# Optimization experiments

Measured on AMD Instinct MI355X. Metric: run time of the kernel, lower is better.

Reference implementation:

```python
import jax, jax.numpy as jnp
import numpy as np


def setup_inputs() -> dict:
    key = jax.random.key(0)
    k1, k2 = jax.random.split(key)
    B, HW, C, M, P = 8, 4096, 1024, 32, 512
    feature_map = jax.random.normal(k1, (B, HW, C), dtype=jnp.float32)
    # normalized (y, x) coords in [0,1], as produced by mask.nonzero()/[H,W]
    point_coords = jax.random.uniform(k2, (B, M, P, 2), dtype=jnp.float32)
    return {"feature_map": feature_map, "point_coords": point_coords}


def reference(feature_map, point_coords):
    # feature_map: [B, H*W, C]; point_coords: [B, M, P, 2] as (y_norm, x_norm).
    B, HW, C = feature_map.shape
    h = w = int(np.sqrt(HW))
    # torch flips coords to (x, y); grid_sample(align_corners=True) maps
    # grid g = 2*coord-1 to pixel coord*(size-1).
    y = point_coords[..., 0] * (h - 1)  # [B, M, P]
    x = point_coords[..., 1] * (w - 1)
    x0f = jnp.floor(x)
    y0f = jnp.floor(y)
    wx = (x - x0f)[..., None]  # [B, M, P, 1]
    wy = (y - y0f)[..., None]
    ix0 = jnp.clip(x0f.astype(jnp.int32), 0, w - 1)
    ix1 = jnp.clip(ix0 + 1, 0, w - 1)
    iy0 = jnp.clip(y0f.astype(jnp.int32), 0, h - 1)
    iy1 = jnp.clip(iy0 + 1, 0, h - 1)

    def gather(iy, ix):
        idx = (iy * w + ix).reshape(B, -1)  # [B, M*P]
        g = jnp.take_along_axis(feature_map, idx[:, :, None], axis=1)  # [B, M*P, C]
        return g.reshape(B, iy.shape[1], iy.shape[2], C)

    f00 = gather(iy0, ix0)
    f01 = gather(iy0, ix1)
    f10 = gather(iy1, ix0)
    f11 = gather(iy1, ix1)
    # bilinear interpolation -> [B, M, P, C]
    sampled = (f00 * (1 - wx) * (1 - wy) + f01 * wx * (1 - wy)
               + f10 * (1 - wx) * wy + f11 * wx * wy)
    # AdaptiveAvgPool1d(1) over points, then transpose -> [B, M, 1, C]
    region_feat = jnp.mean(sampled, axis=2, keepdims=True)
    return region_feat
```

## Files before the change

### kernel.cpp

```cpp
#include <hip/hip_runtime.h>


#define NB 8
#define NM 32
#define NP 512
#define NC 1024
#define NH 64
#define NHW 4096

#define KC   256
#define NKC  (NHW / KC)
#define CT   256
#define NCT  (NC / CT)
#define PF   8

__global__ __launch_bounds__(256) void scatter_w(
    const float* __restrict__ pc, float* __restrict__ W)
{
    int idx = blockIdx.x * 256 + threadIdx.x;
    int bm  = idx >> 9;
    int m   = bm & (NM - 1);
    int b   = bm >> 5;

    float2 c = ((const float2*)pc)[idx];
    float y = c.x * 63.0f;
    float x = c.y * 63.0f;
    float x0f = floorf(x), y0f = floorf(y);
    float wx = x - x0f, wy = y - y0f;
    int ix0 = min(max((int)x0f, 0), 63);
    int ix1 = min(ix0 + 1, 63);
    int iy0 = min(max((int)y0f, 0), 63);
    int iy1 = min(iy0 + 1, 63);
    float wx1 = 1.0f - wx, wy1 = 1.0f - wy;
    const float s = 1.0f / (float)NP;

    float* Wb = W + (size_t)b * (NHW * NM) + m;
    atomicAdd(Wb + ((iy0 * NH + ix0) * NM), wx1 * wy1 * s);
    atomicAdd(Wb + ((iy0 * NH + ix1) * NM), wx  * wy1 * s);
    atomicAdd(Wb + ((iy1 * NH + ix0) * NM), wx1 * wy  * s);
    atomicAdd(Wb + ((iy1 * NH + ix1) * NM), wx  * wy  * s);
}

__global__ __launch_bounds__(256, 2) void wgemm(
    const float* __restrict__ W, const float* __restrict__ F,
    float* __restrict__ P)
{
    __shared__ float4 sW[KC * NM / 4];

    const int kc  = blockIdx.x;
    const int ct  = blockIdx.y;
    const int b   = blockIdx.z;
    const int tid = threadIdx.x;
    const int c   = ct * CT + tid;
    const int hw0 = kc * KC;

    const float4* Wg = (const float4*)(W + ((size_t)b * NHW + hw0) * NM);
#pragma unroll
    for (int j = 0; j < 8; ++j)
        sW[tid + 256 * j] = Wg[tid + 256 * j];
    __syncthreads();

    const float* Fb = F + ((size_t)b * NHW + hw0) * NC + c;

    float acc[NM];
#pragma unroll
    for (int m = 0; m < NM; ++m) acc[m] = 0.0f;

    float fbuf[PF];
#pragma unroll
    for (int j = 0; j < PF; ++j) fbuf[j] = Fb[(size_t)j * NC];

    for (int i = 0; i < KC; i += PF) {
        float fcur[PF];
#pragma unroll
        for (int j = 0; j < PF; ++j) fcur[j] = fbuf[j];
        if (i + PF < KC) {
#pragma unroll
            for (int j = 0; j < PF; ++j)
                fbuf[j] = Fb[(size_t)(i + PF + j) * NC];
        }
#pragma unroll
        for (int j = 0; j < PF; ++j) {
            const float4* w4 = sW + (i + j) * (NM / 4);
            float f = fcur[j];
#pragma unroll
            for (int mq = 0; mq < NM / 4; ++mq) {
                float4 w = w4[mq];
                acc[mq * 4 + 0] = fmaf(w.x, f, acc[mq * 4 + 0]);
                acc[mq * 4 + 1] = fmaf(w.y, f, acc[mq * 4 + 1]);
                acc[mq * 4 + 2] = fmaf(w.z, f, acc[mq * 4 + 2]);
                acc[mq * 4 + 3] = fmaf(w.w, f, acc[mq * 4 + 3]);
            }
        }
    }

    float* pb = P + (((size_t)kc * NB + b) * NM) * NC + c;
#pragma unroll
    for (int m = 0; m < NM; ++m)
        pb[(size_t)m * NC] = acc[m];
}

__global__ __launch_bounds__(256) void reduce_p(
    const float* __restrict__ P, float* __restrict__ out)
{
    const int idx = blockIdx.x * 256 + threadIdx.x;
    const float4* p4 = (const float4*)P;
    const int stride = NB * NM * NC / 4;
    float4 s = make_float4(0.f, 0.f, 0.f, 0.f);
#pragma unroll
    for (int kc = 0; kc < NKC; ++kc) {
        float4 v = p4[(size_t)kc * stride + idx];
        s.x += v.x; s.y += v.y; s.z += v.z; s.w += v.w;
    }
    ((float4*)out)[idx] = s;
}

__global__ __launch_bounds__(256) void region_pool_direct(
    const float* __restrict__ fm, const float* __restrict__ pc,
    float* __restrict__ out)
{
    __shared__ int4   sIdx[NP];
    __shared__ float4 sWt[NP];
    const int bid = blockIdx.x;
    const int b   = bid >> 5;
    const int tid = threadIdx.x;
    const float2* pc2 = (const float2*)(pc + (size_t)bid * NP * 2);
    for (int p = tid; p < NP; p += 256) {
        float2 c = pc2[p];
        float y = c.x * 63.0f, x = c.y * 63.0f;
        float x0f = floorf(x), y0f = floorf(y);
        float wx = x - x0f, wy = y - y0f;
        int ix0 = min(max((int)x0f, 0), 63);
        int ix1 = min(ix0 + 1, 63);
        int iy0 = min(max((int)y0f, 0), 63);
        int iy1 = min(iy0 + 1, 63);
        sIdx[p] = make_int4((iy0 * NH + ix0) << 10, (iy0 * NH + ix1) << 10,
                            (iy1 * NH + ix0) << 10, (iy1 * NH + ix1) << 10);
        float wx1 = 1.0f - wx, wy1 = 1.0f - wy;
        sWt[p] = make_float4(wx1 * wy1, wx * wy1, wx1 * wy, wx * wy);
    }
    __syncthreads();
    const float* Fb = fm + (size_t)b * (NHW * NC) + tid * 4;
    float4 acc = make_float4(0.f, 0.f, 0.f, 0.f);
#pragma unroll 4
    for (int p = 0; p < NP; ++p) {
        int4 off = sIdx[p]; float4 w = sWt[p];
        float4 f00 = *(const float4*)(Fb + off.x);
        float4 f01 = *(const float4*)(Fb + off.y);
        float4 f10 = *(const float4*)(Fb + off.z);
        float4 f11 = *(const float4*)(Fb + off.w);
        acc.x = fmaf(w.x, f00.x, fmaf(w.y, f01.x, fmaf(w.z, f10.x, fmaf(w.w, f11.x, acc.x))));
        acc.y = fmaf(w.x, f00.y, fmaf(w.y, f01.y, fmaf(w.z, f10.y, fmaf(w.w, f11.y, acc.y))));
        acc.z = fmaf(w.x, f00.z, fmaf(w.y, f01.z, fmaf(w.z, f10.z, fmaf(w.w, f11.z, acc.z))));
        acc.w = fmaf(w.x, f00.w, fmaf(w.y, f01.w, fmaf(w.z, f10.w, fmaf(w.w, f11.w, acc.w))));
    }
    const float inv = 1.0f / (float)NP;
    ((float4*)(out + (size_t)bid * NC))[tid] =
        make_float4(acc.x * inv, acc.y * inv, acc.z * inv, acc.w * inv);
}

extern "C" void kernel_launch(void* const* d_in, const int* in_sizes, int n_in,
                              void* d_out, int out_size, void* d_ws, size_t ws_size,
                              hipStream_t stream) {
    const float* fm = (const float*)d_in[0];
    const float* pc = (const float*)d_in[1];
    float* out = (float*)d_out;

    const size_t wbytes = (size_t)NB * NHW * NM * sizeof(float);
    const size_t pbytes = (size_t)NKC * NB * NM * NC * sizeof(float);
    if (ws_size >= wbytes + pbytes) {
        float* W = (float*)d_ws;
        float* P = (float*)((char*)d_ws + wbytes);
        hipMemsetAsync(W, 0, wbytes, stream);
        scatter_w<<<(NB * NM * NP) / 256, 256, 0, stream>>>(pc, W);
        dim3 grid(NKC, NCT, NB);
        wgemm<<<grid, CT, 0, stream>>>(W, fm, P);
        reduce_p<<<(NB * NM * NC / 4) / 256, 256, 0, stream>>>(P, out);
    } else {
        region_pool_direct<<<NB * NM, 256, 0, stream>>>(fm, pc, out);
    }
}
```

Before: 233.1 us.

## Retile wgemm into per-wave 8x8 register tiles with float4 feature loads

Restructures the weighted-GEMM kernel so each wave owns 8 regions and each thread accumulates 8 channels via two float4 loads. Feature reads move from scalar to vectorized loads, and the weight reads per FMA from LDS fall. The HW chunk shrinks to 128 with a deeper occupancy hint, which doubles the partial sums that reduce_p must combine. Each block's four waves now re-read the same feature rows, relying on cache.

```diff
diff --git a/kernel.cpp b/kernel.cpp
--- a/kernel.cpp
+++ b/kernel.cpp
@@ -8,11 +8,10 @@
 #define NH 64
 #define NHW 4096
 
-#define KC   256
+#define KC   128
 #define NKC  (NHW / KC)
-#define CT   256
-#define NCT  (NC / CT)
-#define PF   8
+#define NCT  2
+#define PF   2
 
 __global__ __launch_bounds__(256) void scatter_w(
     const float* __restrict__ pc, float* __restrict__ W)
@@ -41,63 +40,136 @@
     atomicAdd(Wb + ((iy1 * NH + ix1) * NM), wx  * wy  * s);
 }
 
-__global__ __launch_bounds__(256, 2) void wgemm(
+__global__ __launch_bounds__(256, 4) void wgemm(
     const float* __restrict__ W, const float* __restrict__ F,
     float* __restrict__ P)
 {
     __shared__ float4 sW[KC * NM / 4];
 
-    const int kc  = blockIdx.x;
-    const int ct  = blockIdx.y;
-    const int b   = blockIdx.z;
-    const int tid = threadIdx.x;
-    const int c   = ct * CT + tid;
-    const int hw0 = kc * KC;
+    const int kc   = blockIdx.x;
+    const int ct   = blockIdx.y;
+    const int b    = blockIdx.z;
+    const int tid  = threadIdx.x;
+    const int wav  = tid >> 6;
+    const int lane = tid & 63;
+    const int c0   = ct * 512 + lane * 4;
+    const int hw0  = kc * KC;
+    const int wq   = wav * 2;
 
     const float4* Wg = (const float4*)(W + ((size_t)b * NHW + hw0) * NM);
 #pragma unroll
-    for (int j = 0; j < 8; ++j)
+    for (int j = 0; j < 4; ++j)
         sW[tid + 256 * j] = Wg[tid + 256 * j];
     __syncthreads();
 
-    const float* Fb = F + ((size_t)b * NHW + hw0) * NC + c;
-
-    float acc[NM];
-#pragma unroll
-    for (int m = 0; m < NM; ++m) acc[m] = 0.0f;
-
-    float fbuf[PF];
-#pragma unroll
-    for (int j = 0; j < PF; ++j) fbuf[j] = Fb[(size_t)j * NC];
+    const float* Fb = F + ((size_t)b * NHW + hw0) * NC + c0;
+
+    float4 acc[8][2];
+#pragma unroll
+    for (int m = 0; m < 8; ++m) {
+        acc[m][0] = make_float4(0.f, 0.f, 0.f, 0.f);
+        acc[m][1] = make_float4(0.f, 0.f, 0.f, 0.f);
+    }
+
+    float4 fb0[PF], fb1[PF];
+#pragma unroll
+    for (int j = 0; j < PF; ++j) {
+        fb0[j] = *(const float4*)(Fb + (size_t)j * NC);
+        fb1[j] = *(const float4*)(Fb + (size_t)j * NC + 256);
+    }
 
     for (int i = 0; i < KC; i += PF) {
-        float fcur[PF];
-#pragma unroll
-        for (int j = 0; j < PF; ++j) fcur[j] = fbuf[j];
-        if (i + PF < KC) {
-#pragma unroll
-            for (int j = 0; j < PF; ++j)
-                fbuf[j] = Fb[(size_t)(i + PF + j) * NC];
+#pragma unroll
+        for (int j = 0; j < PF; ++j) {
+            float4 f0 = fb0[j], f1 = fb1[j];
+            int inx = i + PF + j;
+            if (inx < KC) {
+                fb0[j] = *(const float4*)(Fb + (size_t)inx * NC);
+                fb1[j] = *(const float4*)(Fb + (size_t)inx * NC + 256);
+            }
+            float4 wa = sW[(i + j) * 8 + wq];
+            float4 wb = sW[(i + j) * 8 + wq + 1];
+
+            acc[0][0].x = fmaf(wa.x, f0.x, acc[0][0].x);
+            acc[0][0].y = fmaf(wa.x, f0.y, acc[0][0].y);
+            acc[0][0].z = fmaf(wa.x, f0.z, acc[0][0].z);
+            acc[0][0].w = fmaf(wa.x, f0.w, acc[0][0].w);
+            acc[0][1].x = fmaf(wa.x, f1.x, acc[0][1].x);
+            acc[0][1].y = fmaf(wa.x, f1.y, acc[0][1].y);
+            acc[0][1].z = fmaf(wa.x, f1.z, acc[0][1].z);
+            acc[0][1].w = fmaf(wa.x, f1.w, acc[0][1].w);
+
+            acc[1][0].x = fmaf(wa.y, f0.x, acc[1][0].x);
+            acc[1][0].y = fmaf(wa.y, f0.y, acc[1][0].y);
+            acc[1][0].z = fmaf(wa.y, f0.z, acc[1][0].z);
+            acc[1][0].w = fmaf(wa.y, f0.w, acc[1][0].w);
+            acc[1][1].x = fmaf(wa.y, f1.x, acc[1][1].x);
+            acc[1][1].y = fmaf(wa.y, f1.y, acc[1][1].y);
+            acc[1][1].z = fmaf(wa.y, f1.z, acc[1][1].z);
+            acc[1][1].w = fmaf(wa.y, f1.w, acc[1][1].w);
+
+            acc[2][0].x = fmaf(wa.z, f0.x, acc[2][0].x);
+            acc[2][0].y = fmaf(wa.z, f0.y, acc[2][0].y);
+            acc[2][0].z = fmaf(wa.z, f0.z, acc[2][0].z);
+            acc[2][0].w = fmaf(wa.z, f0.w, acc[2][0].w);
+            acc[2][1].x = fmaf(wa.z, f1.x, acc[2][1].x);
+            acc[2][1].y = fmaf(wa.z, f1.y, acc[2][1].y);
+            acc[2][1].z = fmaf(wa.z, f1.z, acc[2][1].z);
+            acc[2][1].w = fmaf(wa.z, f1.w, acc[2][1].w);
+
+            acc[3][0].x = fmaf(wa.w, f0.x, acc[3][0].x);
+            acc[3][0].y = fmaf(wa.w, f0.y, acc[3][0].y);
+            acc[3][0].z = fmaf(wa.w, f0.z, acc[3][0].z);
+            acc[3][0].w = fmaf(wa.w, f0.w, acc[3][0].w);
+            acc[3][1].x = fmaf(wa.w, f1.x, acc[3][1].x);
+            acc[3][1].y = fmaf(wa.w, f1.y, acc[3][1].y);
+            acc[3][1].z = fmaf(wa.w, f1.z, acc[3][1].z);
+            acc[3][1].w = fmaf(wa.w, f1.w, acc[3][1].w);
+
+            acc[4][0].x = fmaf(wb.x, f0.x, acc[4][0].x);
+            acc[4][0].y = fmaf(wb.x, f0.y, acc[4][0].y);
+            acc[4][0].z = fmaf(wb.x, f0.z, acc[4][0].z);
+            acc[4][0].w = fmaf(wb.x, f0.w, acc[4][0].w);
+            acc[4][1].x = fmaf(wb.x, f1.x, acc[4][1].x);
+            acc[4][1].y = fmaf(wb.x, f1.y, acc[4][1].y);
+            acc[4][1].z = fmaf(wb.x, f1.z, acc[4][1].z);
+            acc[4][1].w = fmaf(wb.x, f1.w, acc[4][1].w);
+
+            acc[5][0].x = fmaf(wb.y, f0.x, acc[5][0].x);
+            acc[5][0].y = fmaf(wb.y, f0.y, acc[5][0].y);
+            acc[5][0].z = fmaf(wb.y, f0.z, acc[5][0].z);
+            acc[5][0].w = fmaf(wb.y, f0.w, acc[5][0].w);
+            acc[5][1].x = fmaf(wb.y, f1.x, acc[5][1].x);
+            acc[5][1].y = fmaf(wb.y, f1.y, acc[5][1].y);
+            acc[5][1].z = fmaf(wb.y, f1.z, acc[5][1].z);
+            acc[5][1].w = fmaf(wb.y, f1.w, acc[5][1].w);
+
+            acc[6][0].x = fmaf(wb.z, f0.x, acc[6][0].x);
+            acc[6][0].y = fmaf(wb.z, f0.y, acc[6][0].y);
+            acc[6][0].z = fmaf(wb.z, f0.z, acc[6][0].z);
+            acc[6][0].w = fmaf(wb.z, f0.w, acc[6][0].w);
+            acc[6][1].x = fmaf(wb.z, f1.x, acc[6][1].x);
+            acc[6][1].y = fmaf(wb.z, f1.y, acc[6][1].y);
+            acc[6][1].z = fmaf(wb.z, f1.z, acc[6][1].z);
+            acc[6][1].w = fmaf(wb.z, f1.w, acc[6][1].w);
+
+            acc[7][0].x = fmaf(wb.w, f0.x, acc[7][0].x);
+            acc[7][0].y = fmaf(wb.w, f0.y, acc[7][0].y);
+            acc[7][0].z = fmaf(wb.w, f0.z, acc[7][0].z);
+            acc[7][0].w = fmaf(wb.w, f0.w, acc[7][0].w);
+            acc[7][1].x = fmaf(wb.w, f1.x, acc[7][1].x);
+            acc[7][1].y = fmaf(wb.w, f1.y, acc[7][1].y);
+            acc[7][1].z = fmaf(wb.w, f1.z, acc[7][1].z);
+            acc[7][1].w = fmaf(wb.w, f1.w, acc[7][1].w);
         }
-#pragma unroll
-        for (int j = 0; j < PF; ++j) {
-            const float4* w4 = sW + (i + j) * (NM / 4);
-            float f = fcur[j];
-#pragma unroll
-            for (int mq = 0; mq < NM / 4; ++mq) {
-                float4 w = w4[mq];
-                acc[mq * 4 + 0] = fmaf(w.x, f, acc[mq * 4 + 0]);
-                acc[mq * 4 + 1] = fmaf(w.y, f, acc[mq * 4 + 1]);
-                acc[mq * 4 + 2] = fmaf(w.z, f, acc[mq * 4 + 2]);
-                acc[mq * 4 + 3] = fmaf(w.w, f, acc[mq * 4 + 3]);
-            }
-        }
-    }
-
-    float* pb = P + (((size_t)kc * NB + b) * NM) * NC + c;
-#pragma unroll
-    for (int m = 0; m < NM; ++m)
-        pb[(size_t)m * NC] = acc[m];
+    }
+
+    float* pb = P + (((size_t)kc * NB + b) * NM + wav * 8) * NC + c0;
+#pragma unroll
+    for (int m = 0; m < 8; ++m) {
+        *(float4*)(pb + (size_t)m * NC)       = acc[m][0];
+        *(float4*)(pb + (size_t)m * NC + 256) = acc[m][1];
+    }
 }
 
 __global__ __launch_bounds__(256) void reduce_p(
@@ -174,7 +246,7 @@
         hipMemsetAsync(W, 0, wbytes, stream);
         scatter_w<<<(NB * NM * NP) / 256, 256, 0, stream>>>(pc, W);
         dim3 grid(NKC, NCT, NB);
-        wgemm<<<grid, CT, 0, stream>>>(W, fm, P);
+        wgemm<<<grid, 256, 0, stream>>>(W, fm, P);
         reduce_p<<<(NB * NM * NC / 4) / 256, 256, 0, stream>>>(P, out);
     } else {
         region_pool_direct<<<NB * NM, 256, 0, stream>>>(fm, pc, out);
```

Result: slower. 271.6 us (+16.5%).

## Restructure weight GEMM with async LDS double-buffering and 8x8 register tiles

Applied to the files above, without the earlier changes.

The wgemm kernel now copies feature rows and weights straight into LDS with global_load_lds, double-buffers the feature tiles across k-steps, and gives each thread an 8-channel by 8-region register tile instead of one channel by 32 regions. It also doubles the number of k-chunks, changes the channel tiling to two 512-wide tiles, and raises occupancy hints to 3 blocks. The aim is better data reuse per LDS read and load latency hidden behind the FMAs. In exchange the partial-sum buffer doubles in size, which adds reduce traffic and a larger workspace requirement. Correctness also depends on the async LDS loads being complete at the barriers.

```diff
diff --git a/kernel.cpp b/kernel.cpp
--- a/kernel.cpp
+++ b/kernel.cpp
@@ -1,4 +1,5 @@
 #include <hip/hip_runtime.h>
+#include <stdint.h>
 
 
 #define NB 8
@@ -8,11 +9,19 @@
 #define NH 64
 #define NHW 4096
 
-#define KC   256
-#define NKC  (NHW / KC)
-#define CT   256
-#define NCT  (NC / CT)
-#define PF   8
+#define NKC  32
+#define ROWS (NHW / NKC)
+#define KT   8
+#define NT   (ROWS / KT)
+#define NCT  2
+#define CTW  512
+
+__device__ __forceinline__ void async16(const void* g, void* l) {
+    __builtin_amdgcn_global_load_lds(
+        (const __attribute__((address_space(1))) unsigned int*)g,
+        (__attribute__((address_space(3))) unsigned int*)l,
+        16, 0, 0);
+}
 
 __global__ __launch_bounds__(256) void scatter_w(
     const float* __restrict__ pc, float* __restrict__ W)
@@ -41,63 +50,88 @@
     atomicAdd(Wb + ((iy1 * NH + ix1) * NM), wx  * wy  * s);
 }
 
-__global__ __launch_bounds__(256, 2) void wgemm(
+__global__ __launch_bounds__(256, 3) void wgemm(
     const float* __restrict__ W, const float* __restrict__ F,
     float* __restrict__ P)
 {
-    __shared__ float4 sW[KC * NM / 4];
-
-    const int kc  = blockIdx.x;
-    const int ct  = blockIdx.y;
-    const int b   = blockIdx.z;
-    const int tid = threadIdx.x;
-    const int c   = ct * CT + tid;
-    const int hw0 = kc * KC;
-
-    const float4* Wg = (const float4*)(W + ((size_t)b * NHW + hw0) * NM);
-#pragma unroll
-    for (int j = 0; j < 8; ++j)
-        sW[tid + 256 * j] = Wg[tid + 256 * j];
+    __shared__ float4 sF[2][KT * CTW / 4];
+    __shared__ float4 sWt[ROWS * NM / 4];
+
+    const int kc   = blockIdx.x;
+    const int ct   = blockIdx.y;
+    const int b    = blockIdx.z;
+    const int tid  = threadIdx.x;
+    const int wav  = tid >> 6;
+    const int lane = tid & 63;
+    const int hw0  = kc * ROWS;
+    const int wq   = wav * 2;
+    const int c0   = ct * CTW + lane * 4;
+
+    const char* Wg = (const char*)(W + ((size_t)b * NHW + hw0) * NM);
+    const char* Fg = (const char*)(F + ((size_t)b * NHW + hw0) * NC + ct * CTW);
+    const int lane16 = lane * 16;
+
+    {
+        char* lds = (char*)sWt;
+#pragma unroll
+        for (int i = 0; i < 4; ++i) {
+            int j = wav * 4 + i;
+            async16(Wg + j * 1024 + lane16, lds + j * 1024 + lane16);
+        }
+    }
+    auto stage_f = [&](int t, int buf) {
+        char* lds = (char*)sF[buf];
+#pragma unroll
+        for (int i = 0; i < 4; ++i) {
+            int j   = wav * 4 + i;
+            int row = j >> 1, half = j & 1;
+            async16(Fg + (size_t)(t * KT + row) * (NC * 4) + half * 1024 + lane16,
+                    lds + j * 1024 + lane16);
+        }
+    };
+
+    stage_f(0, 0);
     __syncthreads();
 
-    const float* Fb = F + ((size_t)b * NHW + hw0) * NC + c;
-
-    float acc[NM];
-#pragma unroll
-    for (int m = 0; m < NM; ++m) acc[m] = 0.0f;
-
-    float fbuf[PF];
-#pragma unroll
-    for (int j = 0; j < PF; ++j) fbuf[j] = Fb[(size_t)j * NC];
-
-    for (int i = 0; i < KC; i += PF) {
-        float fcur[PF];
-#pragma unroll
-        for (int j = 0; j < PF; ++j) fcur[j] = fbuf[j];
-        if (i + PF < KC) {
-#pragma unroll
-            for (int j = 0; j < PF; ++j)
-                fbuf[j] = Fb[(size_t)(i + PF + j) * NC];
-        }
-#pragma unroll
-        for (int j = 0; j < PF; ++j) {
-            const float4* w4 = sW + (i + j) * (NM / 4);
-            float f = fcur[j];
-#pragma unroll
-            for (int mq = 0; mq < NM / 4; ++mq) {
-                float4 w = w4[mq];
-                acc[mq * 4 + 0] = fmaf(w.x, f, acc[mq * 4 + 0]);
-                acc[mq * 4 + 1] = fmaf(w.y, f, acc[mq * 4 + 1]);
-                acc[mq * 4 + 2] = fmaf(w.z, f, acc[mq * 4 + 2]);
-                acc[mq * 4 + 3] = fmaf(w.w, f, acc[mq * 4 + 3]);
+    float4 acc[8][2];
+#pragma unroll
+    for (int m = 0; m < 8; ++m) {
+        acc[m][0] = make_float4(0.f, 0.f, 0.f, 0.f);
+        acc[m][1] = make_float4(0.f, 0.f, 0.f, 0.f);
+    }
+
+    for (int t = 0; t < NT; ++t) {
+        if (t + 1 < NT) stage_f(t + 1, (t + 1) & 1);
+        const float4* fb   = sF[t & 1];
+        const float4* wrow = sWt + (size_t)(t * KT) * (NM / 4);
+#pragma unroll
+        for (int r = 0; r < KT; ++r) {
+            float4 f0 = fb[r * 128 + lane];
+            float4 f1 = fb[r * 128 + 64 + lane];
+            float4 wa = wrow[r * 8 + wq];
+            float4 wb = wrow[r * 8 + wq + 1];
+            float wv[8] = {wa.x, wa.y, wa.z, wa.w, wb.x, wb.y, wb.z, wb.w};
+#pragma unroll
+            for (int m = 0; m < 8; ++m) {
+                acc[m][0].x = fmaf(wv[m], f0.x, acc[m][0].x);
+                acc[m][0].y = fmaf(wv[m], f0.y, acc[m][0].y);
+                acc[m][0].z = fmaf(wv[m], f0.z, acc[m][0].z);
+                acc[m][0].w = fmaf(wv[m], f0.w, acc[m][0].w);
+                acc[m][1].x = fmaf(wv[m], f1.x, acc[m][1].x);
+                acc[m][1].y = fmaf(wv[m], f1.y, acc[m][1].y);
+                acc[m][1].z = fmaf(wv[m], f1.z, acc[m][1].z);
+                acc[m][1].w = fmaf(wv[m], f1.w, acc[m][1].w);
             }
         }
-    }
-
-    float* pb = P + (((size_t)kc * NB + b) * NM) * NC + c;
-#pragma unroll
-    for (int m = 0; m < NM; ++m)
-        pb[(size_t)m * NC] = acc[m];
+        __syncthreads();
+    }
+
+    float* pb = P + (((size_t)kc * NB + b) * NM + wav * 8) * NC + c0;
+#pragma unroll
+    for (int m = 0; m < 8; ++m) {
+        *(float4*)(pb + (size_t)m * NC)       = acc[m][0];
+        *(float4*)(pb + (size_t)m * NC + 256) = acc[m][1];
+    }
 }
 
 __global__ __launch_bounds__(256) void reduce_p(
@@ -120,7 +154,7 @@
     float* __restrict__ out)
 {
     __shared__ int4   sIdx[NP];
-    __shared__ float4 sWt[NP];
+    __shared__ float4 sWv[NP];
     const int bid = blockIdx.x;
     const int b   = bid >> 5;
     const int tid = threadIdx.x;
@@ -137,14 +171,14 @@
         sIdx[p] = make_int4((iy0 * NH + ix0) << 10, (iy0 * NH + ix1) << 10,
                             (iy1 * NH + ix0) << 10, (iy1 * NH + ix1) << 10);
         float wx1 = 1.0f - wx, wy1 = 1.0f - wy;
-        sWt[p] = make_float4(wx1 * wy1, wx * wy1, wx1 * wy, wx * wy);
+        sWv[p] = make_float4(wx1 * wy1, wx * wy1, wx1 * wy, wx * wy);
     }
     __syncthreads();
     const float* Fb = fm + (size_t)b * (NHW * NC) + tid * 4;
     float4 acc = make_float4(0.f, 0.f, 0.f, 0.f);
 #pragma unroll 4
     for (int p = 0; p < NP; ++p) {
-        int4 off = sIdx[p]; float4 w = sWt[p];
+        int4 off = sIdx[p]; float4 w = sWv[p];
         float4 f00 = *(const float4*)(Fb + off.x);
         float4 f01 = *(const float4*)(Fb + off.y);
         float4 f10 = *(const float4*)(Fb + off.z);
@@ -174,7 +208,7 @@
         hipMemsetAsync(W, 0, wbytes, stream);
         scatter_w<<<(NB * NM * NP) / 256, 256, 0, stream>>>(pc, W);
         dim3 grid(NKC, NCT, NB);
-        wgemm<<<grid, CT, 0, stream>>>(W, fm, P);
+        wgemm<<<grid, 256, 0, stream>>>(W, fm, P);
         reduce_p<<<(NB * NM * NC / 4) / 256, 256, 0, stream>>>(P, out);
     } else {
         region_pool_direct<<<NB * NM, 256, 0, stream>>>(fm, pc, out);
```

Result: slower. 245.6 us (+5.4%).
